# Kernel tuning notes

Hardware: AMD Instinct MI355X
Metric: run time of the kernel (lower is better)

The kernel has to match this reference:

```python
import jax, jax.numpy as jnp
import numpy as np

N = 8192
D = 512


def setup_inputs() -> dict:
    key = jax.random.key(0)
    k1, k2, k3, k4 = jax.random.split(key, 4)
    U = jax.random.normal(k1, (N, D), dtype=jnp.float32)
    V = jax.random.normal(k2, (N, D), dtype=jnp.float32)
    M = jax.random.normal(k3, (N, N), dtype=jnp.float32)
    W = jax.random.uniform(k4, (N, N), dtype=jnp.float32)
    alpha = jnp.ones((1,), dtype=jnp.float32) * 0.1
    return {"U": U, "V": V, "M": M, "W": W, "alpha": alpha}


def reference(U, V, M, W, alpha):
    # Reconstruction term: sum((U V^T - M)^2)
    recon = U @ V.T                                  # (N, N) GEMM
    part1 = jnp.sum(jnp.square(recon - M))
    # Manifold term in closed form:
    # sum_{i,j} W[i,j] * ||U_i - V_j||^2
    #   = sum_i rowW_i ||U_i||^2 + sum_j colW_j ||V_j||^2 - 2 sum(W * U V^T)
    u_sq = jnp.sum(U * U, axis=1)                    # (N,)
    v_sq = jnp.sum(V * V, axis=1)                    # (N,)
    row_w = jnp.sum(W, axis=1)                       # (N,)
    col_w = jnp.sum(W, axis=0)                       # (N,)
    cross = jnp.sum(W * recon)
    part2 = alpha[0] * (jnp.dot(row_w, u_sq) + jnp.dot(col_w, v_sq) - 2.0 * cross)
    total = part1 + part2
    return total / (M.shape[0] * M.shape[1])
```

## Files before the change

### kernel.cpp

```cpp
#include <hip/hip_runtime.h>
#include <hip/hip_bf16.h>
#include <stdint.h>

#define N_DIM 8192
#define D_DIM 512
#define BM 128
#define BN 128
#define BK 64

typedef __attribute__((ext_vector_type(8))) short bf16x8;
typedef __attribute__((ext_vector_type(4))) float f32x4;

__device__ __forceinline__ unsigned short f2bf(float f) {
    unsigned int x = __float_as_uint(f);
    x += 0x7fffu + ((x >> 16) & 1u);
    return (unsigned short)(x >> 16);
}

__global__ void __launch_bounds__(256) prep_kernel(
    const float* __restrict__ U, const float* __restrict__ V,
    unsigned short* __restrict__ Ub, unsigned short* __restrict__ Vb,
    float* __restrict__ usq, float* __restrict__ vsq)
{
    int row = blockIdx.x;
    const float* src;
    unsigned short* dst;
    float* sq;
    if (row < N_DIM) {
        src = U + (size_t)row * D_DIM;
        dst = Ub + (size_t)row * D_DIM;
        sq  = usq + row;
    } else {
        int r = row - N_DIM;
        src = V + (size_t)r * D_DIM;
        dst = Vb + (size_t)r * D_DIM;
        sq  = vsq + r;
    }
    int t = threadIdx.x;
    float2 v = *reinterpret_cast<const float2*>(src + 2 * t);
    float s = v.x * v.x + v.y * v.y;
    ushort2 b;
    b.x = f2bf(v.x);
    b.y = f2bf(v.y);
    *reinterpret_cast<ushort2*>(dst + 2 * t) = b;

    #pragma unroll
    for (int o = 32; o > 0; o >>= 1) s += __shfl_down(s, o, 64);
    __shared__ float red[4];
    if ((t & 63) == 0) red[t >> 6] = s;
    __syncthreads();
    if (t == 0) *sq = red[0] + red[1] + red[2] + red[3];
}

__global__ void __launch_bounds__(256, 2) fused_kernel(
    const unsigned short* __restrict__ Ub, const unsigned short* __restrict__ Vb,
    const float* __restrict__ Mg, const float* __restrict__ Wg,
    const float* __restrict__ usq, const float* __restrict__ vsq,
    double* __restrict__ acc)
{
    __shared__ alignas(16) char As[BM * BK * 2];
    __shared__ alignas(16) char Bs[BN * BK * 2];
    __shared__ float red1[4], red2[4];

    const int t    = threadIdx.x;
    const int lane = t & 63;
    const int wave = t >> 6;
    const int wm   = wave >> 1;
    const int wn   = wave & 1;

    const int bid    = blockIdx.x;
    const int tile_m = bid >> 6;
    const int tile_n = bid & 63;
    const int row0   = tile_m * BM;
    const int col0   = tile_n * BN;

    const f32x4 zero = {0.f, 0.f, 0.f, 0.f};
    f32x4 acc_r[4][4];
    #pragma unroll
    for (int i = 0; i < 4; ++i)
        #pragma unroll
        for (int j = 0; j < 4; ++j)
            acc_r[i][j] = zero;

    auto As3 = (__attribute__((address_space(3))) char*)As;
    auto Bs3 = (__attribute__((address_space(3))) char*)Bs;

    for (int kt = 0; kt < D_DIM / BK; ++kt) {
        const int k0 = kt * BK;
        #pragma unroll
        for (int c = 0; c < 4; ++c) {
            int s   = c * 256 + t;
            int row = s >> 3;
            int kg  = s & 7;
            int kgs = kg ^ (row & 7);
            const unsigned short* ga = Ub + (size_t)(row0 + row) * D_DIM + k0 + kgs * 8;
            __builtin_amdgcn_global_load_lds(
                (const __attribute__((address_space(1))) void*)ga,
                (__attribute__((address_space(3))) void*)(As3 + s * 16), 16, 0, 0);
            const unsigned short* gb = Vb + (size_t)(col0 + row) * D_DIM + k0 + kgs * 8;
            __builtin_amdgcn_global_load_lds(
                (const __attribute__((address_space(1))) void*)gb,
                (__attribute__((address_space(3))) void*)(Bs3 + s * 16), 16, 0, 0);
        }
        __syncthreads();

        #pragma unroll
        for (int kc = 0; kc < 2; ++kc) {
            bf16x8 af[4], bfr[4];
            const int kgw = kc * 4 + (lane >> 4);
            #pragma unroll
            for (int i = 0; i < 4; ++i) {
                int ra   = wm * 64 + i * 16 + (lane & 15);
                int offa = ra * (BK * 2) + ((kgw ^ (ra & 7)) * 16);
                af[i] = *reinterpret_cast<const bf16x8*>(As + offa);
                int rb   = wn * 64 + i * 16 + (lane & 15);
                int offb = rb * (BK * 2) + ((kgw ^ (rb & 7)) * 16);
                bfr[i] = *reinterpret_cast<const bf16x8*>(Bs + offb);
            }
            #pragma unroll
            for (int i = 0; i < 4; ++i)
                #pragma unroll
                for (int j = 0; j < 4; ++j)
                    acc_r[i][j] = __builtin_amdgcn_mfma_f32_16x16x32_bf16(
                        af[i], bfr[j], acc_r[i][j], 0, 0, 0);
        }
        __syncthreads();
    }

    float us[4][4];
    #pragma unroll
    for (int i = 0; i < 4; ++i) {
        int r0 = row0 + wm * 64 + i * 16 + (lane >> 4) * 4;
        #pragma unroll
        for (int q = 0; q < 4; ++q) us[i][q] = usq[r0 + q];
    }
    float vsn[4];
    #pragma unroll
    for (int j = 0; j < 4; ++j)
        vsn[j] = vsq[col0 + wn * 64 + j * 16 + (lane & 15)];

    float s1 = 0.f, s2 = 0.f;
    #pragma unroll
    for (int i = 0; i < 4; ++i) {
        int rbase = row0 + wm * 64 + i * 16 + (lane >> 4) * 4;
        #pragma unroll
        for (int j = 0; j < 4; ++j) {
            int cidx = col0 + wn * 64 + j * 16 + (lane & 15);
            #pragma unroll
            for (int q = 0; q < 4; ++q) {
                size_t idx = (size_t)(rbase + q) * N_DIM + cidx;
                float rec = acc_r[i][j][q];
                float m   = Mg[idx];
                float w   = Wg[idx];
                float d   = rec - m;
                s1 = fmaf(d, d, s1);
                s2 = fmaf(w, us[i][q] + vsn[j] - 2.f * rec, s2);
            }
        }
    }

    #pragma unroll
    for (int o = 32; o > 0; o >>= 1) {
        s1 += __shfl_down(s1, o, 64);
        s2 += __shfl_down(s2, o, 64);
    }
    if (lane == 0) { red1[wave] = s1; red2[wave] = s2; }
    __syncthreads();
    if (t == 0) {
        double a1 = (double)red1[0] + red1[1] + red1[2] + red1[3];
        double a2 = (double)red2[0] + red2[1] + red2[2] + red2[3];
        atomicAdd(acc, a1);
        atomicAdd(acc + 1, a2);
    }
}

__global__ void finalize_kernel(const double* __restrict__ acc,
                                const float* __restrict__ alpha,
                                float* __restrict__ out)
{
    double tot = acc[0] + (double)alpha[0] * acc[1];
    out[0] = (float)(tot / ((double)N_DIM * (double)N_DIM));
}

extern "C" void kernel_launch(void* const* d_in, const int* in_sizes, int n_in,
                              void* d_out, int out_size, void* d_ws, size_t ws_size,
                              hipStream_t stream) {
    const float* U     = (const float*)d_in[0];
    const float* V     = (const float*)d_in[1];
    const float* Mg    = (const float*)d_in[2];
    const float* Wg    = (const float*)d_in[3];
    const float* alpha = (const float*)d_in[4];

    char* ws = (char*)d_ws;
    unsigned short* Ub = (unsigned short*)ws;
    unsigned short* Vb = (unsigned short*)(ws + 8u * 1024 * 1024);
    float* usq = (float*)(ws + 16u * 1024 * 1024);
    float* vsq = (float*)(ws + 16u * 1024 * 1024 + 32u * 1024);
    double* acc = (double*)(ws + 16u * 1024 * 1024 + 64u * 1024);

    hipMemsetAsync(acc, 0, 2 * sizeof(double), stream);
    prep_kernel<<<2 * N_DIM, 256, 0, stream>>>(U, V, Ub, Vb, usq, vsq);
    fused_kernel<<<(N_DIM / BM) * (N_DIM / BN), 256, 0, stream>>>(
        Ub, Vb, Mg, Wg, usq, vsq, acc);
    finalize_kernel<<<1, 1, 0, stream>>>(acc, alpha, (float*)d_out);
}
```

Baseline: 175.9 us.

## Stage GEMM tile through LDS for coalesced float4 epilogue loads of M and W

The epilogue now writes the MFMA accumulator tile into shared memory in two 64-row halves, reusing the GEMM staging buffer. Each thread then reads M and W with contiguous 16-byte vector loads along rows, instead of scattered 4-byte loads in the MFMA output layout. The block index is remapped so that concurrently scheduled blocks touch different tile rows, and the launch bound is raised to 4 blocks per CU to allow more occupancy. The cost is extra LDS traffic and barriers, plus possible register pressure from the higher occupancy target.

After: 202.4 us. 1.15x slower.

```diff
diff --git a/kernel.cpp b/kernel.cpp
--- a/kernel.cpp
+++ b/kernel.cpp
@@ -52,15 +52,17 @@
     if (t == 0) *sq = red[0] + red[1] + red[2] + red[3];
 }
 
-__global__ void __launch_bounds__(256, 2) fused_kernel(
+__global__ void __launch_bounds__(256, 4) fused_kernel(
     const unsigned short* __restrict__ Ub, const unsigned short* __restrict__ Vb,
     const float* __restrict__ Mg, const float* __restrict__ Wg,
     const float* __restrict__ usq, const float* __restrict__ vsq,
     double* __restrict__ acc)
 {
-    __shared__ alignas(16) char As[BM * BK * 2];
-    __shared__ alignas(16) char Bs[BN * BK * 2];
+    __shared__ alignas(16) char smem[BM * BK * 2 + BN * BK * 2];
     __shared__ float red1[4], red2[4];
+    char* As = smem;
+    char* Bs = smem + BM * BK * 2;
+    float* recs = (float*)smem;
 
     const int t    = threadIdx.x;
     const int lane = t & 63;
@@ -68,7 +70,7 @@
     const int wm   = wave >> 1;
     const int wn   = wave & 1;
 
-    const int bid    = blockIdx.x;
+    const int bid    = (blockIdx.x & 7) * 512 + (blockIdx.x >> 3);
     const int tile_m = bid >> 6;
     const int tile_n = bid & 63;
     const int row0   = tile_m * BM;
@@ -127,36 +129,53 @@
         __syncthreads();
     }
 
-    float us[4][4];
-    #pragma unroll
-    for (int i = 0; i < 4; ++i) {
-        int r0 = row0 + wm * 64 + i * 16 + (lane >> 4) * 4;
-        #pragma unroll
-        for (int q = 0; q < 4; ++q) us[i][q] = usq[r0 + q];
-    }
-    float vsn[4];
-    #pragma unroll
-    for (int j = 0; j < 4; ++j)
-        vsn[j] = vsq[col0 + wn * 64 + j * 16 + (lane & 15)];
+    const int rloc = t >> 5;
+    const int c4   = (t & 31) * 4;
+    const f32x4 vs = *reinterpret_cast<const f32x4*>(vsq + col0 + c4);
 
     float s1 = 0.f, s2 = 0.f;
-    #pragma unroll
-    for (int i = 0; i < 4; ++i) {
-        int rbase = row0 + wm * 64 + i * 16 + (lane >> 4) * 4;
-        #pragma unroll
-        for (int j = 0; j < 4; ++j) {
-            int cidx = col0 + wn * 64 + j * 16 + (lane & 15);
-            #pragma unroll
-            for (int q = 0; q < 4; ++q) {
-                size_t idx = (size_t)(rbase + q) * N_DIM + cidx;
-                float rec = acc_r[i][j][q];
-                float m   = Mg[idx];
-                float w   = Wg[idx];
-                float d   = rec - m;
-                s1 = fmaf(d, d, s1);
-                s2 = fmaf(w, us[i][q] + vsn[j] - 2.f * rec, s2);
+
+    #pragma unroll
+    for (int h = 0; h < 2; ++h) {
+        if (wm == h) {
+            #pragma unroll
+            for (int i = 0; i < 4; ++i)
+                #pragma unroll
+                for (int j = 0; j < 4; ++j)
+                    #pragma unroll
+                    for (int q = 0; q < 4; ++q)
+                        recs[(i * 16 + (lane >> 4) * 4 + q) * 128 +
+                             wn * 64 + j * 16 + (lane & 15)] = acc_r[i][j][q];
+        }
+        __syncthreads();
+
+        const float* Mrow = Mg + (size_t)(row0 + h * 64) * N_DIM + col0 + c4;
+        const float* Wrow = Wg + (size_t)(row0 + h * 64) * N_DIM + col0 + c4;
+
+        #pragma unroll
+        for (int kk = 0; kk < 2; ++kk) {
+            f32x4 mv[4], wv[4];
+            float usr[4];
+            #pragma unroll
+            for (int b = 0; b < 4; ++b) {
+                int r = rloc + (kk * 4 + b) * 8;
+                mv[b]  = *reinterpret_cast<const f32x4*>(Mrow + (size_t)r * N_DIM);
+                wv[b]  = *reinterpret_cast<const f32x4*>(Wrow + (size_t)r * N_DIM);
+                usr[b] = usq[row0 + h * 64 + r];
             }
-        }
+            #pragma unroll
+            for (int b = 0; b < 4; ++b) {
+                int r = rloc + (kk * 4 + b) * 8;
+                f32x4 rc = *reinterpret_cast<const f32x4*>(recs + r * 128 + c4);
+                #pragma unroll
+                for (int c = 0; c < 4; ++c) {
+                    float d = rc[c] - mv[b][c];
+                    s1 = fmaf(d, d, s1);
+                    s2 = fmaf(wv[b][c], usr[b] + vs[c] - 2.f * rc[c], s2);
+                }
+            }
+        }
+        __syncthreads();
     }
 
     #pragma unroll
```

## Overlap M/W epilogue streaming with next tile's GEMM via LDS-staged results

Applied to the files above, without the earlier changes.

Each block now computes four consecutive column tiles. The previous tile's products are dumped as bf16 into LDS, and the M/W reads and reduction for that tile are streamed in 16-row chunks interleaved with the next tile's MFMA k-loop. The goal is to hide the large HBM read of M and W behind tensor compute, where before it was a serialized epilogue. It also switches to coalesced float4 loads. The cost is more LDS (about 66KB per block, likely reducing occupancy), a grid cut by four, and the reconstruction values rounded to bf16 before the error terms, which adds precision loss.

Result: slower. 218.7 us (+24.3%).

```diff
diff --git a/kernel.cpp b/kernel.cpp
--- a/kernel.cpp
+++ b/kernel.cpp
@@ -7,6 +7,8 @@
 #define BM 128
 #define BN 128
 #define BK 64
+#define RSTR 136
+#define TPB 4
 
 typedef __attribute__((ext_vector_type(8))) short bf16x8;
 typedef __attribute__((ext_vector_type(4))) float f32x4;
@@ -15,6 +17,9 @@
     unsigned int x = __float_as_uint(f);
     x += 0x7fffu + ((x >> 16) & 1u);
     return (unsigned short)(x >> 16);
+}
+__device__ __forceinline__ float bf2f(unsigned short u) {
+    return __uint_as_float(((unsigned int)u) << 16);
 }
 
 __global__ void __launch_bounds__(256) prep_kernel(
@@ -58,9 +63,11 @@
     const float* __restrict__ usq, const float* __restrict__ vsq,
     double* __restrict__ acc)
 {
-    __shared__ alignas(16) char As[BM * BK * 2];
-    __shared__ alignas(16) char Bs[BN * BK * 2];
+    __shared__ alignas(16) char smem[BM * BK * 2 + BN * BK * 2];
+    __shared__ alignas(16) unsigned short recs[BM * RSTR];
     __shared__ float red1[4], red2[4];
+    char* As = smem;
+    char* Bs = smem + BM * BK * 2;
 
     const int t    = threadIdx.x;
     const int lane = t & 63;
@@ -69,94 +76,156 @@
     const int wn   = wave & 1;
 
     const int bid    = blockIdx.x;
-    const int tile_m = bid >> 6;
-    const int tile_n = bid & 63;
+    const int tile_m = bid >> 4;
+    const int quad   = bid & 15;
     const int row0   = tile_m * BM;
-    const int col0   = tile_n * BN;
-
-    const f32x4 zero = {0.f, 0.f, 0.f, 0.f};
-    f32x4 acc_r[4][4];
-    #pragma unroll
-    for (int i = 0; i < 4; ++i)
-        #pragma unroll
-        for (int j = 0; j < 4; ++j)
-            acc_r[i][j] = zero;
+
+    const int rg = t >> 4;
+    const int ct = t & 15;
+    const int c8 = ct * 8;
+
+    float s1 = 0.f, s2 = 0.f;
 
     auto As3 = (__attribute__((address_space(3))) char*)As;
     auto Bs3 = (__attribute__((address_space(3))) char*)Bs;
 
-    for (int kt = 0; kt < D_DIM / BK; ++kt) {
-        const int k0 = kt * BK;
+    auto stage = [&](const unsigned short* Ua, const unsigned short* Va, int k0) {
         #pragma unroll
         for (int c = 0; c < 4; ++c) {
             int s   = c * 256 + t;
             int row = s >> 3;
             int kg  = s & 7;
             int kgs = kg ^ (row & 7);
-            const unsigned short* ga = Ub + (size_t)(row0 + row) * D_DIM + k0 + kgs * 8;
             __builtin_amdgcn_global_load_lds(
-                (const __attribute__((address_space(1))) void*)ga,
+                (const __attribute__((address_space(1))) void*)(Ua + (size_t)row * D_DIM + k0 + kgs * 8),
                 (__attribute__((address_space(3))) void*)(As3 + s * 16), 16, 0, 0);
-            const unsigned short* gb = Vb + (size_t)(col0 + row) * D_DIM + k0 + kgs * 8;
             __builtin_amdgcn_global_load_lds(
-                (const __attribute__((address_space(1))) void*)gb,
+                (const __attribute__((address_space(1))) void*)(Va + (size_t)row * D_DIM + k0 + kgs * 8),
                 (__attribute__((address_space(3))) void*)(Bs3 + s * 16), 16, 0, 0);
         }
-        __syncthreads();
-
+    };
+
+    auto mma = [&](f32x4 (&a)[4][4]) {
         #pragma unroll
         for (int kc = 0; kc < 2; ++kc) {
             bf16x8 af[4], bfr[4];
             const int kgw = kc * 4 + (lane >> 4);
             #pragma unroll
             for (int i = 0; i < 4; ++i) {
-                int ra   = wm * 64 + i * 16 + (lane & 15);
-                int offa = ra * (BK * 2) + ((kgw ^ (ra & 7)) * 16);
-                af[i] = *reinterpret_cast<const bf16x8*>(As + offa);
-                int rb   = wn * 64 + i * 16 + (lane & 15);
-                int offb = rb * (BK * 2) + ((kgw ^ (rb & 7)) * 16);
-                bfr[i] = *reinterpret_cast<const bf16x8*>(Bs + offb);
+                int ra = wm * 64 + i * 16 + (lane & 15);
+                af[i]  = *reinterpret_cast<const bf16x8*>(As + ra * (BK * 2) + ((kgw ^ (ra & 7)) * 16));
+                int rb = wn * 64 + i * 16 + (lane & 15);
+                bfr[i] = *reinterpret_cast<const bf16x8*>(Bs + rb * (BK * 2) + ((kgw ^ (rb & 7)) * 16));
             }
             #pragma unroll
             for (int i = 0; i < 4; ++i)
                 #pragma unroll
                 for (int j = 0; j < 4; ++j)
-                    acc_r[i][j] = __builtin_amdgcn_mfma_f32_16x16x32_bf16(
-                        af[i], bfr[j], acc_r[i][j], 0, 0, 0);
-        }
-        __syncthreads();
-    }
-
-    float us[4][4];
+                    a[i][j] = __builtin_amdgcn_mfma_f32_16x16x32_bf16(af[i], bfr[j], a[i][j], 0, 0, 0);
+        }
+    };
+
+    auto dump = [&](f32x4 (&a)[4][4]) {
+        #pragma unroll
+        for (int i = 0; i < 4; ++i)
+            #pragma unroll
+            for (int j = 0; j < 4; ++j)
+                #pragma unroll
+                for (int q = 0; q < 4; ++q) {
+                    int r = wm * 64 + i * 16 + (lane >> 4) * 4 + q;
+                    int c = wn * 64 + j * 16 + (lane & 15);
+                    recs[r * RSTR + c] = f2bf(a[i][j][q]);
+                }
+    };
+
+    int   colp = 0;
+    f32x4 vs0v, vs1v;
+
+    auto issue = [&](int chunk, f32x4& m0, f32x4& m1, f32x4& w0, f32x4& w1, float& us) {
+        int r = chunk * 16 + rg;
+        const float* Mp = Mg + (size_t)(row0 + r) * N_DIM + colp + c8;
+        const float* Wp = Wg + (size_t)(row0 + r) * N_DIM + colp + c8;
+        m0 = *reinterpret_cast<const f32x4*>(Mp);
+        m1 = *reinterpret_cast<const f32x4*>(Mp + 4);
+        w0 = *reinterpret_cast<const f32x4*>(Wp);
+        w1 = *reinterpret_cast<const f32x4*>(Wp + 4);
+        us = usq[row0 + r];
+    };
+
+    auto consume = [&](int chunk, f32x4 m0, f32x4 m1, f32x4 w0, f32x4 w1, float us) {
+        int r = chunk * 16 + rg;
+        bf16x8 rb = *reinterpret_cast<const bf16x8*>(&recs[r * RSTR + c8]);
+        #pragma unroll
+        for (int c = 0; c < 4; ++c) {
+            float rc = bf2f((unsigned short)rb[c]);
+            float d  = rc - m0[c];
+            s1 = fmaf(d, d, s1);
+            s2 = fmaf(w0[c], us + vs0v[c] - 2.f * rc, s2);
+        }
+        #pragma unroll
+        for (int c = 0; c < 4; ++c) {
+            float rc = bf2f((unsigned short)rb[4 + c]);
+            float d  = rc - m1[c];
+            s1 = fmaf(d, d, s1);
+            s2 = fmaf(w1[c], us + vs1v[c] - 2.f * rc, s2);
+        }
+    };
+
+    const f32x4 zero = {0.f, 0.f, 0.f, 0.f};
+    const unsigned short* Ua = Ub + (size_t)row0 * D_DIM;
+
+    f32x4 a[4][4];
+    f32x4 mvA[2], wvA[2], mvB[2], wvB[2];
+    float usA, usB;
+
+    for (int it = 0; it < TPB; ++it) {
+        const int col0 = (quad * TPB + it) * BN;
+        const unsigned short* Va = Vb + (size_t)col0 * D_DIM;
+        const bool strm = (it > 0);
+
+        #pragma unroll
+        for (int i = 0; i < 4; ++i)
+            #pragma unroll
+            for (int j = 0; j < 4; ++j) a[i][j] = zero;
+
+        if (strm) {
+            colp = (quad * TPB + it - 1) * BN;
+            vs0v = *reinterpret_cast<const f32x4*>(vsq + colp + c8);
+            vs1v = *reinterpret_cast<const f32x4*>(vsq + colp + c8 + 4);
+            issue(0, mvA[0], mvA[1], wvA[0], wvA[1], usA);
+        }
+
+        #pragma unroll
+        for (int kt = 0; kt < D_DIM / BK; ++kt) {
+            stage(Ua, Va, kt * BK);
+            __syncthreads();
+            if (strm && kt < 7) {
+                if (kt & 1) issue(kt + 1, mvA[0], mvA[1], wvA[0], wvA[1], usA);
+                else        issue(kt + 1, mvB[0], mvB[1], wvB[0], wvB[1], usB);
+            }
+            mma(a);
+            if (strm) {
+                if (kt & 1) consume(kt, mvB[0], mvB[1], wvB[0], wvB[1], usB);
+                else        consume(kt, mvA[0], mvA[1], wvA[0], wvA[1], usA);
+            }
+            __syncthreads();
+        }
+        dump(a);
+    }
+
+    colp = (quad * TPB + TPB - 1) * BN;
+    vs0v = *reinterpret_cast<const f32x4*>(vsq + colp + c8);
+    vs1v = *reinterpret_cast<const f32x4*>(vsq + colp + c8 + 4);
+    __syncthreads();
+    issue(0, mvA[0], mvA[1], wvA[0], wvA[1], usA);
     #pragma unroll
-    for (int i = 0; i < 4; ++i) {
-        int r0 = row0 + wm * 64 + i * 16 + (lane >> 4) * 4;
-        #pragma unroll
-        for (int q = 0; q < 4; ++q) us[i][q] = usq[r0 + q];
-    }
-    float vsn[4];
-    #pragma unroll
-    for (int j = 0; j < 4; ++j)
-        vsn[j] = vsq[col0 + wn * 64 + j * 16 + (lane & 15)];
-
-    float s1 = 0.f, s2 = 0.f;
-    #pragma unroll
-    for (int i = 0; i < 4; ++i) {
-        int rbase = row0 + wm * 64 + i * 16 + (lane >> 4) * 4;
-        #pragma unroll
-        for (int j = 0; j < 4; ++j) {
-            int cidx = col0 + wn * 64 + j * 16 + (lane & 15);
-            #pragma unroll
-            for (int q = 0; q < 4; ++q) {
-                size_t idx = (size_t)(rbase + q) * N_DIM + cidx;
-                float rec = acc_r[i][j][q];
-                float m   = Mg[idx];
-                float w   = Wg[idx];
-                float d   = rec - m;
-                s1 = fmaf(d, d, s1);
-                s2 = fmaf(w, us[i][q] + vsn[j] - 2.f * rec, s2);
-            }
-        }
+    for (int chunk = 0; chunk < 8; ++chunk) {
+        if (chunk < 7) {
+            if (chunk & 1) issue(chunk + 1, mvA[0], mvA[1], wvA[0], wvA[1], usA);
+            else           issue(chunk + 1, mvB[0], mvB[1], wvB[0], wvB[1], usB);
+        }
+        if (chunk & 1) consume(chunk, mvB[0], mvB[1], wvB[0], wvB[1], usB);
+        else           consume(chunk, mvA[0], mvA[1], wvA[0], wvA[1], usA);
     }
 
     #pragma unroll
@@ -167,10 +236,10 @@
     if (lane == 0) { red1[wave] = s1; red2[wave] = s2; }
     __syncthreads();
     if (t == 0) {
-        double a1 = (double)red1[0] + red1[1] + red1[2] + red1[3];
-        double a2 = (double)red2[0] + red2[1] + red2[2] + red2[3];
-        atomicAdd(acc, a1);
-        atomicAdd(acc + 1, a2);
+        double a1s = (double)red1[0] + red1[1] + red1[2] + red1[3];
+        double a2s = (double)red2[0] + red2[1] + red2[2] + red2[3];
+        atomicAdd(acc, a1s);
+        atomicAdd(acc + 1, a2s);
     }
 }
 
@@ -200,7 +269,7 @@
 
     hipMemsetAsync(acc, 0, 2 * sizeof(double), stream);
     prep_kernel<<<2 * N_DIM, 256, 0, stream>>>(U, V, Ub, Vb, usq, vsq);
-    fused_kernel<<<(N_DIM / BM) * (N_DIM / BN), 256, 0, stream>>>(
+    fused_kernel<<<(N_DIM / BM) * (N_DIM / BN) / TPB, 256, 0, stream>>>(
         Ub, Vb, Mg, Wg, usq, vsq, acc);
     finalize_kernel<<<1, 1, 0, stream>>>(acc, alpha, (float*)d_out);
 }
```

## Stage GEMM tile through LDS for coalesced vectorized M/W epilogue loads

Applied to the files above, without the earlier changes.

The epilogue now writes the GEMM accumulator tile into a padded shared-memory buffer as bf16. Threads then re-read it row-wise so each can load M and W with 128-bit coalesced vector loads, software-pipelined three rows deep. This replaces the previous scattered scalar loads that followed the MFMA output layout. In exchange it rounds the reconstruction to bf16 before the loss terms, which costs accuracy, and it adds about 35KB of LDS per block, which may hurt occupancy.

After: 181.8 us. 1.03x slower.

```diff
diff --git a/kernel.cpp b/kernel.cpp
--- a/kernel.cpp
+++ b/kernel.cpp
@@ -7,6 +7,7 @@
 #define BM 128
 #define BN 128
 #define BK 64
+#define RSTR 140
 
 typedef __attribute__((ext_vector_type(8))) short bf16x8;
 typedef __attribute__((ext_vector_type(4))) float f32x4;
@@ -15,6 +16,9 @@
     unsigned int x = __float_as_uint(f);
     x += 0x7fffu + ((x >> 16) & 1u);
     return (unsigned short)(x >> 16);
+}
+__device__ __forceinline__ float bf2f(unsigned short u) {
+    return __uint_as_float(((unsigned int)u) << 16);
 }
 
 __global__ void __launch_bounds__(256) prep_kernel(
@@ -58,9 +62,11 @@
     const float* __restrict__ usq, const float* __restrict__ vsq,
     double* __restrict__ acc)
 {
-    __shared__ alignas(16) char As[BM * BK * 2];
-    __shared__ alignas(16) char Bs[BN * BK * 2];
+    __shared__ alignas(16) char smem[BM * BK * 2 + BN * BK * 2];
+    __shared__ alignas(16) unsigned short recs[BM * RSTR];
     __shared__ float red1[4], red2[4];
+    char* As = smem;
+    char* Bs = smem + BM * BK * 2;
 
     const int t    = threadIdx.x;
     const int lane = t & 63;
@@ -75,12 +81,11 @@
     const int col0   = tile_n * BN;
 
     const f32x4 zero = {0.f, 0.f, 0.f, 0.f};
-    f32x4 acc_r[4][4];
+    f32x4 a[4][4];
     #pragma unroll
     for (int i = 0; i < 4; ++i)
         #pragma unroll
-        for (int j = 0; j < 4; ++j)
-            acc_r[i][j] = zero;
+        for (int j = 0; j < 4; ++j) a[i][j] = zero;
 
     auto As3 = (__attribute__((address_space(3))) char*)As;
     auto Bs3 = (__attribute__((address_space(3))) char*)Bs;
@@ -93,13 +98,11 @@
             int row = s >> 3;
             int kg  = s & 7;
             int kgs = kg ^ (row & 7);
-            const unsigned short* ga = Ub + (size_t)(row0 + row) * D_DIM + k0 + kgs * 8;
             __builtin_amdgcn_global_load_lds(
-                (const __attribute__((address_space(1))) void*)ga,
+                (const __attribute__((address_space(1))) void*)(Ub + (size_t)(row0 + row) * D_DIM + k0 + kgs * 8),
                 (__attribute__((address_space(3))) void*)(As3 + s * 16), 16, 0, 0);
-            const unsigned short* gb = Vb + (size_t)(col0 + row) * D_DIM + k0 + kgs * 8;
             __builtin_amdgcn_global_load_lds(
-                (const __attribute__((address_space(1))) void*)gb,
+                (const __attribute__((address_space(1))) void*)(Vb + (size_t)(col0 + row) * D_DIM + k0 + kgs * 8),
                 (__attribute__((address_space(3))) void*)(Bs3 + s * 16), 16, 0, 0);
         }
         __syncthreads();
@@ -110,52 +113,79 @@
             const int kgw = kc * 4 + (lane >> 4);
             #pragma unroll
             for (int i = 0; i < 4; ++i) {
-                int ra   = wm * 64 + i * 16 + (lane & 15);
-                int offa = ra * (BK * 2) + ((kgw ^ (ra & 7)) * 16);
-                af[i] = *reinterpret_cast<const bf16x8*>(As + offa);
-                int rb   = wn * 64 + i * 16 + (lane & 15);
-                int offb = rb * (BK * 2) + ((kgw ^ (rb & 7)) * 16);
-                bfr[i] = *reinterpret_cast<const bf16x8*>(Bs + offb);
+                int ra = wm * 64 + i * 16 + (lane & 15);
+                af[i]  = *reinterpret_cast<const bf16x8*>(As + ra * (BK * 2) + ((kgw ^ (ra & 7)) * 16));
+                int rb = wn * 64 + i * 16 + (lane & 15);
+                bfr[i] = *reinterpret_cast<const bf16x8*>(Bs + rb * (BK * 2) + ((kgw ^ (rb & 7)) * 16));
             }
             #pragma unroll
             for (int i = 0; i < 4; ++i)
                 #pragma unroll
                 for (int j = 0; j < 4; ++j)
-                    acc_r[i][j] = __builtin_amdgcn_mfma_f32_16x16x32_bf16(
-                        af[i], bfr[j], acc_r[i][j], 0, 0, 0);
+                    a[i][j] = __builtin_amdgcn_mfma_f32_16x16x32_bf16(af[i], bfr[j], a[i][j], 0, 0, 0);
         }
         __syncthreads();
     }
 
-    float us[4][4];
-    #pragma unroll
-    for (int i = 0; i < 4; ++i) {
-        int r0 = row0 + wm * 64 + i * 16 + (lane >> 4) * 4;
-        #pragma unroll
-        for (int q = 0; q < 4; ++q) us[i][q] = usq[r0 + q];
-    }
-    float vsn[4];
-    #pragma unroll
-    for (int j = 0; j < 4; ++j)
-        vsn[j] = vsq[col0 + wn * 64 + j * 16 + (lane & 15)];
+    const int rg = t >> 4;
+    const int c8 = (t & 15) * 8;
+
+    const f32x4 vs0 = *reinterpret_cast<const f32x4*>(vsq + col0 + c8);
+    const f32x4 vs1 = *reinterpret_cast<const f32x4*>(vsq + col0 + c8 + 4);
 
     float s1 = 0.f, s2 = 0.f;
-    #pragma unroll
-    for (int i = 0; i < 4; ++i) {
-        int rbase = row0 + wm * 64 + i * 16 + (lane >> 4) * 4;
-        #pragma unroll
-        for (int j = 0; j < 4; ++j) {
-            int cidx = col0 + wn * 64 + j * 16 + (lane & 15);
+
+    f32x4 m0[3], m1[3], w0[3], w1[3];
+    float us[3];
+
+    auto issue = [&](int chunk, int slot) {
+        int r = chunk * 16 + rg;
+        const float* Mp = Mg + (size_t)(row0 + r) * N_DIM + col0 + c8;
+        const float* Wp = Wg + (size_t)(row0 + r) * N_DIM + col0 + c8;
+        m0[slot] = *reinterpret_cast<const f32x4*>(Mp);
+        m1[slot] = *reinterpret_cast<const f32x4*>(Mp + 4);
+        w0[slot] = *reinterpret_cast<const f32x4*>(Wp);
+        w1[slot] = *reinterpret_cast<const f32x4*>(Wp + 4);
+        us[slot] = usq[row0 + r];
+    };
+
+    issue(0, 0);
+    issue(1, 1);
+    issue(2, 2);
+
+    #pragma unroll
+    for (int i = 0; i < 4; ++i)
+        #pragma unroll
+        for (int j = 0; j < 4; ++j)
             #pragma unroll
             for (int q = 0; q < 4; ++q) {
-                size_t idx = (size_t)(rbase + q) * N_DIM + cidx;
-                float rec = acc_r[i][j][q];
-                float m   = Mg[idx];
-                float w   = Wg[idx];
-                float d   = rec - m;
-                s1 = fmaf(d, d, s1);
-                s2 = fmaf(w, us[i][q] + vsn[j] - 2.f * rec, s2);
+                int r = wm * 64 + i * 16 + (lane >> 4) * 4 + q;
+                int c = wn * 64 + j * 16 + (lane & 15);
+                recs[r * RSTR + c] = f2bf(a[i][j][q]);
             }
+    __syncthreads();
+
+    #pragma unroll
+    for (int chunk = 0; chunk < 8; ++chunk) {
+        const int slot = chunk % 3;
+        int r = chunk * 16 + rg;
+        bf16x8 rb = *reinterpret_cast<const bf16x8*>(&recs[r * RSTR + c8]);
+        f32x4 lm0 = m0[slot], lm1 = m1[slot], lw0 = w0[slot], lw1 = w1[slot];
+        float lus = us[slot];
+        if (chunk + 3 < 8) issue(chunk + 3, slot);
+        #pragma unroll
+        for (int c = 0; c < 4; ++c) {
+            float rc = bf2f((unsigned short)rb[c]);
+            float d  = rc - lm0[c];
+            s1 = fmaf(d, d, s1);
+            s2 = fmaf(lw0[c], lus + vs0[c] - 2.f * rc, s2);
+        }
+        #pragma unroll
+        for (int c = 0; c < 4; ++c) {
+            float rc = bf2f((unsigned short)rb[4 + c]);
+            float d  = rc - lm1[c];
+            s1 = fmaf(d, d, s1);
+            s2 = fmaf(lw1[c], lus + vs1[c] - 2.f * rc, s2);
         }
     }
 
@@ -167,10 +197,10 @@
     if (lane == 0) { red1[wave] = s1; red2[wave] = s2; }
     __syncthreads();
     if (t == 0) {
-        double a1 = (double)red1[0] + red1[1] + red1[2] + red1[3];
-        double a2 = (double)red2[0] + red2[1] + red2[2] + red2[3];
-        atomicAdd(acc, a1);
-        atomicAdd(acc + 1, a2);
+        double a1s = (double)red1[0] + red1[1] + red1[2] + red1[3];
+        double a2s = (double)red2[0] + red2[1] + red2[2] + red2[3];
+        atomicAdd(acc, a1s);
+        atomicAdd(acc + 1, a2s);
     }
 }
 
```
